# Optimization experiments

Measured on AMD Instinct MI355X. Metric: run time of the kernel, lower is better.

## Reference

```python
import jax, jax.numpy as jnp
import numpy as np
from jax import lax

VOCAB, E, H = 32000, 256, 512
B, T = 64, 1024


def setup_inputs() -> dict:
    key = jax.random.key(0)
    ks = jax.random.split(key, 5)
    tokens = jax.random.randint(ks[0], (B, T), 0, VOCAB, dtype=jnp.int64 if jax.config.jax_enable_x64 else jnp.int32).astype(jnp.int32)
    emb_table = jax.random.normal(ks[1], (VOCAB, E), dtype=jnp.float32) * 0.02
    W_x = jax.random.normal(ks[2], (E, 4 * H), dtype=jnp.float32) * 0.02
    W_h = jax.random.normal(ks[3], (H, 4 * H), dtype=jnp.float32) * 0.02
    b = jnp.zeros((4 * H,), dtype=jnp.float32)
    h0 = jnp.zeros((B, H), dtype=jnp.float32)
    c0 = jnp.zeros((B, H), dtype=jnp.float32)
    return {"tokens": tokens, "h0": h0, "c0": c0, "emb_table": emb_table,
            "W_x": W_x, "W_h": W_h, "b": b}


def reference(tokens, h0, c0, emb_table, W_x, W_h, b):
    # Embedding lookup with mask_zero=True semantics: token 0 is padding.
    x = emb_table[tokens]                      # [B, T, E]
    mask = tokens != 0                         # [B, T]
    # Precompute input projections for all timesteps (same math, one GEMM).
    xz = jnp.einsum('bte,ef->btf', x, W_x) + b  # [B, T, 4H]

    def step(carry, inp):
        h, c = carry
        xzt, mt = inp                          # [B,4H], [B]
        z = xzt + h @ W_h                      # [B, 4H]
        i, f, g, o = jnp.split(z, 4, axis=-1)  # Keras gate order: i, f, c, o
        i = jax.nn.sigmoid(i)
        f = jax.nn.sigmoid(f)
        g = jnp.tanh(g)
        o = jax.nn.sigmoid(o)
        c_new = f * c + i * g
        h_new = o * jnp.tanh(c_new)
        m = mt[:, None]
        # Masked steps carry previous state/output (Keras masking behavior).
        h = jnp.where(m, h_new, h)
        c = jnp.where(m, c_new, c)
        return (h, c), h

    (h_T, c_T), outs = lax.scan(step, (h0, c0),
                                (xz.transpose(1, 0, 2), mask.T))
    return outs.transpose(1, 0, 2), h_T, c_T  # [B,T,H], [B,H], [B,H]
```

## Files before the change

kernel.cpp:

```cpp
#include <hip/hip_runtime.h>
#include <hip/hip_bf16.h>

#define B_ 64
#define T_ 1024
#define E_ 256
#define H_ 512
#define ZN_ 2048
#define NSLICE 64
#define KT_ 24

typedef short bf16x8 __attribute__((ext_vector_type(8)));
typedef float f32x4 __attribute__((ext_vector_type(4)));
typedef int i32x4 __attribute__((ext_vector_type(4)));

union frag_u { i32x4 i; bf16x8 h; };

__device__ __forceinline__ short f2bf(float f) {
  union { float f; unsigned u; } v; v.f = f;
  unsigned r = v.u + 0x7fffu + ((v.u >> 16) & 1u);
  return (short)(r >> 16);
}
__device__ __forceinline__ float sigmoidf_(float x) {
  return 1.f / (1.f + __expf(-x));
}
__device__ __forceinline__ float tanhf_(float x) {
  x = fminf(10.f, fmaxf(-10.f, x));
  float e = __expf(2.f * x);
  return (e - 1.f) / (e + 1.f);
}

__device__ __forceinline__ i32x4 ld_sys(const void* p) {
  i32x4 r;
  asm volatile("global_load_dwordx4 %0, %1, off sc0 sc1" : "=v"(r) : "v"(p) : "memory");
  return r;
}
__device__ __forceinline__ void st_sys(void* p, i32x4 v) {
  asm volatile("global_store_dwordx4 %0, %1, off sc0 sc1" :: "v"(p), "v"(v) : "memory");
}


__global__ void k_emb_cvt(const float* __restrict__ emb, short* __restrict__ dst, int n8) {
  int i = blockIdx.x * blockDim.x + threadIdx.x;
  if (i >= n8) return;
  const float4* s = (const float4*)emb;
  float4 a = s[2 * i], b = s[2 * i + 1];
  bf16x8 o;
  o[0] = f2bf(a.x); o[1] = f2bf(a.y); o[2] = f2bf(a.z); o[3] = f2bf(a.w);
  o[4] = f2bf(b.x); o[5] = f2bf(b.y); o[6] = f2bf(b.z); o[7] = f2bf(b.w);
  ((bf16x8*)dst)[i] = o;
}

__global__ void k_wfrag(const float* __restrict__ Wx, const float* __restrict__ Wh,
                        short* __restrict__ wf) {
  int tid = blockIdx.x * blockDim.x + threadIdx.x;
  if (tid >= NSLICE * 2 * KT_ * 64) return;
  int lane = tid & 63;
  int kt = (tid >> 6) % KT_;
  int nt = (tid >> 6) / KT_ % 2;
  int s = tid / (64 * KT_ * 2);
  int c16 = lane & 15, ksub = lane >> 4;
  int g = c16 & 3, hc = c16 >> 2;
  int zcol = g * H_ + s * 8 + nt * 4 + hc;
  int k0 = kt * 32 + ksub * 8;
  bf16x8 o;
#pragma unroll
  for (int i = 0; i < 8; ++i) {
    int k = k0 + i;
    float v = (k < E_) ? Wx[(size_t)k * ZN_ + zcol] : Wh[(size_t)(k - E_) * ZN_ + zcol];
    o[i] = f2bf(v);
  }
  ((bf16x8*)wf)[tid] = o;
}

__global__ void k_tok(const int* __restrict__ tok, int* __restrict__ tokT,
                      unsigned long long* __restrict__ mask) {
  int t = blockIdx.x * blockDim.x + threadIdx.x;
  if (t >= T_) return;
  unsigned long long m = 0ull;
  for (int b = 0; b < B_; ++b) {
    int tk = tok[b * T_ + t];
    tokT[t * B_ + b] = tk;
    if (tk != 0) m |= (1ull << b);
  }
  mask[t] = m;
}

__global__ void k_init(const float* __restrict__ h0, short* __restrict__ hbuf0,
                       unsigned* __restrict__ cnt) {
  int i = blockIdx.x * blockDim.x + threadIdx.x;
  if (i == 0) *cnt = 0u;
  if (i >= B_ * H_) return;
  hbuf0[i] = f2bf(h0[i]);
}


__global__ __launch_bounds__(512) void k_lstm(
    const int* __restrict__ tokT, const short* __restrict__ emb,
    const short* __restrict__ wf, const float* __restrict__ bias,
    const unsigned long long* __restrict__ maskv,
    short* __restrict__ hb0, short* __restrict__ hb1,
    const float* __restrict__ h0, const float* __restrict__ c0,
    float* __restrict__ out, unsigned* __restrict__ cnt)
{
  __shared__ __align__(16) float hlocF[B_][8];
  __shared__ __align__(16) short hlocBF[B_][8];

  int s = blockIdx.x;
  int w = threadIdx.x >> 6, l = threadIdx.x & 63;
  int mtile = w & 3, ntile = w >> 2;
  int c16 = l & 15, ksub = l >> 4;
  int g = c16 & 3, hc = c16 >> 2;
  int arow = mtile * 16 + c16;
  int lcol = ntile * 4 + hc;
  int col = s * 8 + lcol;

  bf16x8 wreg[KT_];
  {
    const bf16x8* bp = (const bf16x8*)wf + ((size_t)(s * 2 + ntile) * KT_) * 64 + l;
#pragma unroll
    for (int kt = 0; kt < KT_; ++kt) wreg[kt] = bp[kt * 64];
  }
  float zb = bias[g * H_ + col];

  float cst[4], hst[4];
#pragma unroll
  for (int r = 0; r < 4; ++r) {
    int row = mtile * 16 + ksub * 4 + r;
    cst[r] = c0[row * H_ + col];
    hst[r] = h0[row * H_ + col];
  }

  auto compute_x = [&](int t) -> f32x4 {
    int tk = tokT[t * B_ + arow];
    const bf16x8* ax = (const bf16x8*)emb + (size_t)tk * 32 + ksub;
    f32x4 a0 = {0.f, 0.f, 0.f, 0.f}, a1 = {0.f, 0.f, 0.f, 0.f};
#pragma unroll
    for (int kt = 0; kt < 8; kt += 2) {
      a0 = __builtin_amdgcn_mfma_f32_16x16x32_bf16(ax[kt * 4], wreg[kt], a0, 0, 0, 0);
      a1 = __builtin_amdgcn_mfma_f32_16x16x32_bf16(ax[(kt + 1) * 4], wreg[kt + 1], a1, 0, 0, 0);
    }
    return a0 + a1;
  };

  f32x4 accx = compute_x(0);

  for (int t = 0; t < T_; ++t) {
    const short* hr = (t & 1) ? hb1 : hb0;
    short* hw       = (t & 1) ? hb0 : hb1;

    if (t > 0) {
      if (threadIdx.x == 0) {
        unsigned target = (unsigned)t * NSLICE;
        while (__hip_atomic_load(cnt, __ATOMIC_RELAXED, __HIP_MEMORY_SCOPE_AGENT) < target)
          __builtin_amdgcn_s_sleep(1);
      }
      __syncthreads();
    }

    const short* hbase = hr + arow * H_ + ksub * 8;
    frag_u hf[16];
#pragma unroll
    for (int kt = 0; kt < 16; ++kt)
      hf[kt].i = ld_sys(hbase + kt * 32);
    asm volatile("s_waitcnt vmcnt(0)" ::: "memory");
    __builtin_amdgcn_sched_barrier(0);

    f32x4 acc = accx;
    f32x4 b0 = {0.f, 0.f, 0.f, 0.f};
#pragma unroll
    for (int kt = 0; kt < 16; kt += 2) {
      acc = __builtin_amdgcn_mfma_f32_16x16x32_bf16(hf[kt].h, wreg[8 + kt], acc, 0, 0, 0);
      b0  = __builtin_amdgcn_mfma_f32_16x16x32_bf16(hf[kt + 1].h, wreg[9 + kt], b0, 0, 0, 0);
    }
    acc += b0;

    float act[4];
#pragma unroll
    for (int r = 0; r < 4; ++r) {
      float z = acc[r] + zb;
      act[r] = (g == 2) ? tanhf_(z) : sigmoidf_(z);
    }

    unsigned long long mk = maskv[t];
    int base = l & ~3;
#pragma unroll
    for (int r = 0; r < 4; ++r) {
      float fs = __shfl(act[r], base + 1);
      float gt = __shfl(act[r], base + 2);
      float os = __shfl(act[r], base + 3);
      if (g == 0) {
        int row = mtile * 16 + ksub * 4 + r;
        bool mm = (mk >> row) & 1ull;
        float cn = fs * cst[r] + act[r] * gt;
        float hn = os * tanhf_(cn);
        if (mm) { cst[r] = cn; hst[r] = hn; }
        hlocF[row][lcol] = hst[r];
        hlocBF[row][lcol] = f2bf(hst[r]);
      }
    }
    if (t == T_ - 1 && g == 0) {
#pragma unroll
      for (int r = 0; r < 4; ++r) {
        int row = mtile * 16 + ksub * 4 + r;
        out[(size_t)B_ * T_ * H_ + row * H_ + col] = hst[r];
        out[(size_t)B_ * T_ * H_ + B_ * H_ + row * H_ + col] = cst[r];
      }
    }
    __syncthreads();

    {
      int tid = threadIdx.x;
      if (tid < 64) {
        frag_u v; v.h = *(const bf16x8*)&hlocBF[tid][0];
        st_sys(hw + tid * H_ + s * 8, v.i);
      }
      if (tid < 128) {
        int row = tid >> 1, half = tid & 1;
        f32x4 v = *(const f32x4*)&hlocF[row][half * 4];
        __builtin_nontemporal_store(v, (f32x4*)(out + ((size_t)row * T_ + t) * H_ + s * 8 + half * 4));
      }
    }
    asm volatile("s_waitcnt vmcnt(0)" ::: "memory");
    __syncthreads();
    if (threadIdx.x == 0)
      __hip_atomic_fetch_add(cnt, 1u, __ATOMIC_RELAXED, __HIP_MEMORY_SCOPE_AGENT);

    if (t + 1 < T_) accx = compute_x(t + 1);
  }
}


extern "C" void kernel_launch(void* const* d_in, const int* in_sizes, int n_in,
                              void* d_out, int out_size, void* d_ws, size_t ws_size,
                              hipStream_t stream) {
  (void)in_sizes; (void)n_in; (void)out_size; (void)ws_size;
  const int* tokens = (const int*)d_in[0];
  const float* h0 = (const float*)d_in[1];
  const float* c0 = (const float*)d_in[2];
  const float* emb = (const float*)d_in[3];
  const float* Wx = (const float*)d_in[4];
  const float* Wh = (const float*)d_in[5];
  const float* bias = (const float*)d_in[6];
  float* out = (float*)d_out;
  char* ws = (char*)d_ws;

  short* emb_bf = (short*)(ws);
  short* wf     = (short*)(ws + 16384000);
  unsigned long long* mask = (unsigned long long*)(ws + 19529728);
  int* tokT     = (int*)(ws + 19537920);
  short* hb0    = (short*)(ws + 19800064);
  short* hb1    = (short*)(ws + 19800064 + 65536);
  unsigned* cnt = (unsigned*)(ws + 19931136);

  k_emb_cvt<<<(1024000 + 255) / 256, 256, 0, stream>>>(emb, emb_bf, 1024000);
  k_wfrag<<<(NSLICE * 2 * KT_ * 64 + 255) / 256, 256, 0, stream>>>(Wx, Wh, wf);
  k_tok<<<(T_ + 255) / 256, 256, 0, stream>>>(tokens, tokT, mask);
  k_init<<<(B_ * H_ + 255) / 256, 256, 0, stream>>>(h0, hb0, cnt);

  k_lstm<<<NSLICE, 512, 0, stream>>>(tokT, emb_bf, wf, bias, mask,
                                     hb0, hb1, h0, c0, out, cnt);
}
```

Measured before the change: 7.635 ms.

## Replace atomic counter barrier with per-block flags polled by every wave

The shared atomic counter grid barrier is replaced with per-block step flags. Each block writes its own padded flag after storing its h slice, and every wave polls all 64 flags in parallel, one per lane, then proceeds when all show the current step. This removes the atomic contention and the block-wide syncthreads broadcast after the spin. Output writes now go directly from registers, so the second syncthreads and the output store no longer sit on the path before the flag is published. The cost is more polling traffic, since every wave polls 64 flags instead of one thread polling one counter.

```diff
diff --git a/kernel.cpp b/kernel.cpp
--- a/kernel.cpp
+++ b/kernel.cpp
@@ -36,6 +36,15 @@
 }
 __device__ __forceinline__ void st_sys(void* p, i32x4 v) {
   asm volatile("global_store_dwordx4 %0, %1, off sc0 sc1" :: "v"(p), "v"(v) : "memory");
+}
+__device__ __forceinline__ int ld_sys_poll(const int* p) {
+  int r;
+  asm volatile("global_load_dword %0, %1, off sc0 sc1\n\ts_waitcnt vmcnt(0)"
+               : "=v"(r) : "v"(p) : "memory");
+  return r;
+}
+__device__ __forceinline__ void st_sys_i32(int* p, int v) {
+  asm volatile("global_store_dword %0, %1, off sc0 sc1" :: "v"(p), "v"(v) : "memory");
 }
 
 
@@ -86,9 +95,9 @@
 }
 
 __global__ void k_init(const float* __restrict__ h0, short* __restrict__ hbuf0,
-                       unsigned* __restrict__ cnt) {
+                       int* __restrict__ flags) {
   int i = blockIdx.x * blockDim.x + threadIdx.x;
-  if (i == 0) *cnt = 0u;
+  if (i < 1024) flags[i] = 0;
   if (i >= B_ * H_) return;
   hbuf0[i] = f2bf(h0[i]);
 }
@@ -100,9 +109,8 @@
     const unsigned long long* __restrict__ maskv,
     short* __restrict__ hb0, short* __restrict__ hb1,
     const float* __restrict__ h0, const float* __restrict__ c0,
-    float* __restrict__ out, unsigned* __restrict__ cnt)
+    float* __restrict__ out, int* __restrict__ flags)
 {
-  __shared__ __align__(16) float hlocF[B_][8];
   __shared__ __align__(16) short hlocBF[B_][8];
 
   int s = blockIdx.x;
@@ -113,6 +121,7 @@
   int arow = mtile * 16 + c16;
   int lcol = ntile * 4 + hc;
   int col = s * 8 + lcol;
+  const int* myflag = flags + l * 16;
 
   bf16x8 wreg[KT_];
   {
@@ -149,12 +158,11 @@
     short* hw       = (t & 1) ? hb0 : hb1;
 
     if (t > 0) {
-      if (threadIdx.x == 0) {
-        unsigned target = (unsigned)t * NSLICE;
-        while (__hip_atomic_load(cnt, __ATOMIC_RELAXED, __HIP_MEMORY_SCOPE_AGENT) < target)
-          __builtin_amdgcn_s_sleep(1);
-      }
-      __syncthreads();
+      for (;;) {
+        int v = ld_sys_poll(myflag);
+        if (__all(v >= t)) break;
+        __builtin_amdgcn_s_sleep(1);
+      }
     }
 
     const short* hbase = hr + arow * H_ + ksub * 8;
@@ -194,8 +202,24 @@
         float cn = fs * cst[r] + act[r] * gt;
         float hn = os * tanhf_(cn);
         if (mm) { cst[r] = cn; hst[r] = hn; }
-        hlocF[row][lcol] = hst[r];
         hlocBF[row][lcol] = f2bf(hst[r]);
+      }
+    }
+
+    __syncthreads();
+
+    if (w == 0) {
+      frag_u v; v.h = *(const bf16x8*)&hlocBF[l][0];
+      st_sys(hw + l * H_ + s * 8, v.i);
+      asm volatile("s_waitcnt vmcnt(0)" ::: "memory");
+      if (l == 0) st_sys_i32((int*)(flags + s * 16), t + 1);
+    }
+
+    if (g == 0) {
+#pragma unroll
+      for (int r = 0; r < 4; ++r) {
+        int row = mtile * 16 + ksub * 4 + r;
+        __builtin_nontemporal_store(hst[r], out + ((size_t)row * T_ + t) * H_ + col);
       }
     }
     if (t == T_ - 1 && g == 0) {
@@ -206,24 +230,6 @@
         out[(size_t)B_ * T_ * H_ + B_ * H_ + row * H_ + col] = cst[r];
       }
     }
-    __syncthreads();
-
-    {
-      int tid = threadIdx.x;
-      if (tid < 64) {
-        frag_u v; v.h = *(const bf16x8*)&hlocBF[tid][0];
-        st_sys(hw + tid * H_ + s * 8, v.i);
-      }
-      if (tid < 128) {
-        int row = tid >> 1, half = tid & 1;
-        f32x4 v = *(const f32x4*)&hlocF[row][half * 4];
-        __builtin_nontemporal_store(v, (f32x4*)(out + ((size_t)row * T_ + t) * H_ + s * 8 + half * 4));
-      }
-    }
-    asm volatile("s_waitcnt vmcnt(0)" ::: "memory");
-    __syncthreads();
-    if (threadIdx.x == 0)
-      __hip_atomic_fetch_add(cnt, 1u, __ATOMIC_RELAXED, __HIP_MEMORY_SCOPE_AGENT);
 
     if (t + 1 < T_) accx = compute_x(t + 1);
   }
@@ -250,13 +256,13 @@
   int* tokT     = (int*)(ws + 19537920);
   short* hb0    = (short*)(ws + 19800064);
   short* hb1    = (short*)(ws + 19800064 + 65536);
-  unsigned* cnt = (unsigned*)(ws + 19931136);
+  int* flags    = (int*)(ws + 19931136);
 
   k_emb_cvt<<<(1024000 + 255) / 256, 256, 0, stream>>>(emb, emb_bf, 1024000);
   k_wfrag<<<(NSLICE * 2 * KT_ * 64 + 255) / 256, 256, 0, stream>>>(Wx, Wh, wf);
   k_tok<<<(T_ + 255) / 256, 256, 0, stream>>>(tokens, tokT, mask);
-  k_init<<<(B_ * H_ + 255) / 256, 256, 0, stream>>>(h0, hb0, cnt);
+  k_init<<<(B_ * H_ + 255) / 256, 256, 0, stream>>>(h0, hb0, flags);
 
   k_lstm<<<NSLICE, 512, 0, stream>>>(tokT, emb_bf, wf, bias, mask,
-                                     hb0, hb1, h0, c0, out, cnt);
-}
+                                     hb0, hb1, h0, c0, out, flags);
+}
```

Measured after the change: 7.511 ms. Within noise of the previous version (-1.6%).
